# Kernel tuning notes

Measured on AMD Instinct MI355X. Metric: run time of the kernel, lower is better.

Reference implementation:

```python
import jax, jax.numpy as jnp
import numpy as np
from jax import lax

DT = 1.0 / 120.0      # system dt from SystemModel(dt=1/120)
G = 9.81              # gravity for friction force
K_SIGN = 100.0        # smooth sign() sharpness (tanh surrogate, differentiable)
TWO_PI = 2.0 * np.pi


def setup_inputs() -> dict:
    key = jax.random.key(0)
    k1, k2, k3, k4 = jax.random.split(key, 4)
    N, T = 8192, 64
    params = jax.random.uniform(k1, (4,), jnp.float32, 0.05, 0.5)           # friction, damping, tableRes, rimFriction
    covariance_params = jax.random.normal(k2, (7,), jnp.float32) * 0.5 - 5.0  # log-variances
    init_state = jax.random.normal(k3, (N, 6), jnp.float32) * 0.5            # [x, y, vx, vy, theta, omega]
    measurements = jax.random.normal(k4, (N, T, 3), jnp.float32) * 0.5       # [x, y, theta] per step
    return {"params": params, "covariance_params": covariance_params,
            "init_state": init_state, "measurements": measurements}


def reference(params, covariance_params, init_state, measurements):
    """Batched EKF over N segments (vectorized over the Python segment loop of the
    original) with lax.scan over the segment_size timesteps. Returns the mean
    log-likelihood loss: mean over segments of sum_t 0.5*(logdet(S_t) + y_t^T S_t^{-1} y_t),
    with the +-2*pi angle-wrap on the theta innovation as in the original."""
    dyna = jnp.abs(params)
    fric, damp = dyna[0], dyna[1]

    cp = covariance_params
    R = jnp.diag(jnp.exp(cp[:3]))                                            # 3x3 measurement noise
    Q = jnp.diag(jnp.exp(jnp.stack([cp[3], cp[3], cp[4], cp[4], cp[5], cp[6]])))  # 6x6 process noise

    N = init_state.shape[0]
    P0 = jnp.broadcast_to(jnp.eye(6, dtype=init_state.dtype) * 0.01, (N, 6, 6))
    midx = jnp.array([0, 1, 4])
    H = jnp.zeros((3, 6), init_state.dtype).at[0, 0].set(1.).at[1, 1].set(1.).at[2, 4].set(1.)
    I6 = jnp.eye(6, dtype=init_state.dtype)

    def predict(x):
        # free-slide puck dynamics: damping + dry friction (smooth sign)
        pos, vel, th, om = x[:, 0:2], x[:, 2:4], x[:, 4], x[:, 5]
        t = jnp.tanh(K_SIGN * vel)
        pos_n = pos + DT * vel
        vel_n = vel - DT * (damp * vel + fric * G * t)
        th_n = th + DT * om
        om_n = om - DT * damp * om
        return jnp.concatenate([pos_n, vel_n, th_n[:, None], om_n[:, None]], axis=1), t

    def jacobian_F(t):
        # analytic Jacobian of predict; [N,6,6]
        N_ = t.shape[0]
        dv = 1.0 - DT * (damp + fric * G * K_SIGN * (1.0 - t * t))           # [N,2]
        F = jnp.broadcast_to(I6, (N_, 6, 6))
        F = F.at[:, 0, 2].set(DT).at[:, 1, 3].set(DT).at[:, 4, 5].set(DT)
        F = F.at[:, 2, 2].set(dv[:, 0]).at[:, 3, 3].set(dv[:, 1])
        F = F.at[:, 5, 5].set(1.0 - DT * damp)
        return F

    def step(carry, z):
        x, P = carry
        x_pred, t = predict(x)
        F = jacobian_F(t)
        P_pred = jnp.einsum('nij,njk,nlk->nil', F, P, F) + Q                  # F P F^T + Q

        y = z - x_pred[:, midx]                                               # innovation [N,3]
        ang = y[:, 2]
        ang = jnp.where(ang > 1.5 * np.pi, ang - TWO_PI,
                        jnp.where(ang < -1.5 * np.pi, ang + TWO_PI, ang))
        y = y.at[:, 2].set(ang)

        S = P_pred[:, midx, :][:, :, midx] + R                                # [N,3,3]
        Sinv = jnp.linalg.inv(S)
        K = jnp.einsum('nij,njk->nik', P_pred[:, :, midx], Sinv)              # [N,6,3]

        x_new = x_pred + jnp.einsum('nij,nj->ni', K, y)
        KH = jnp.einsum('nij,jk->nik', K, H)                                  # [N,6,6]
        P_new = jnp.einsum('nij,njk->nik', I6 - KH, P_pred)

        _, logdet = jnp.linalg.slogdet(S)
        maha = jnp.einsum('ni,nij,nj->n', y, Sinv, y)
        loss_t = 0.5 * jnp.sum(logdet + maha)
        return (x_new, P_new), loss_t

    (_, _), losses = lax.scan(step, (init_state, P0),
                              jnp.transpose(measurements, (1, 0, 2)))        # scan over T
    return jnp.sum(losses) / N
```

## Files before the change

### kernel.cpp

```cpp
#include <hip/hip_runtime.h>
#include <math.h>

#define DT_STEP (1.0f / 120.0f)
#define G_ACC 9.81f
#define KS 100.0f

__device__ __forceinline__ float frcp(float x) { return __builtin_amdgcn_rcpf(x); }

template <int FT>
__device__ __forceinline__ void ekf_step(
    const float damp, const float fG, const float a55,
    const float R, const float Qp, const float Qv,
    float& s0, float& s1, float& a, float& b, float& c,
    const float z, float& maha, float& sprod)
{
    const float PI15 = 4.7123889803846899f;
    const float TWOPI = 6.2831853071795865f;

    float s0p, s1p, dv;
    if constexpr (FT < 2) {
        const float e = __expf(2.0f * KS * s1);
        const float u = 2.0f * frcp(e + 1.0f);
        const float th = 1.0f - u;
        s0p = fmaf(DT_STEP, s1, s0);
        s1p = s1 - DT_STEP * fmaf(damp, s1, fG * th);
        dv = 1.0f - DT_STEP * fmaf(fG * KS, u * (2.0f - u), damp);
    } else {
        s0p = fmaf(DT_STEP, s1, s0);
        s1p = a55 * s1;
        dv = a55;
    }

    const float M00 = fmaf(DT_STEP, b, a);
    const float M01 = fmaf(DT_STEP, c, b);
    const float Pp00 = fmaf(DT_STEP, M01, M00) + Qp;
    const float Pp01 = dv * M01;
    const float Pp11 = fmaf(dv * dv, c, Qv);

    float y = z - s0p;
    if constexpr (FT == 2) {
        if (y > PI15) y -= TWOPI;
        else if (y < -PI15) y += TWOPI;
    }

    const float S = Pp00 + R;
    const float Si = frcp(S);
    const float K0 = Pp00 * Si;
    const float K1 = Pp01 * Si;

    s0 = fmaf(K0, y, s0p);
    s1 = fmaf(K1, y, s1p);

    const float omk = 1.0f - K0;
    a = Pp00 * omk;
    b = Pp01 * omk;
    c = fmaf(-K1, Pp01, Pp11);

    maha = fmaf(y * y, Si, maha);
    sprod *= S;
}

template <int TT, int FT>
__device__ __forceinline__ float run_filter(
    const float damp, const float fG, const float a55,
    const float R, const float Qp, const float Qv,
    float s0, float s1, const float (&z)[TT])
{
    float a = 0.01f, b = 0.0f, c = 0.01f;
    float maha = 0.0f, logsum = 0.0f;
    static_assert(TT % 8 == 0, "TT multiple of 8");
#pragma unroll
    for (int g = 0; g < TT / 8; g++) {
        float sprod = 1.0f;
#pragma unroll
        for (int k = 0; k < 8; k++)
            ekf_step<FT>(damp, fG, a55, R, Qp, Qv, s0, s1, a, b, c, z[g * 8 + k], maha, sprod);
        logsum += __logf(sprod);
    }
    return logsum + maha;
}

template <int TT>
__global__ __launch_bounds__(64, 1) void ekf_reg_kernel(
    const float* __restrict__ params, const float* __restrict__ cp,
    const float* __restrict__ init_state, const float* __restrict__ meas,
    float* __restrict__ out, int N)
{
    const int lane = threadIdx.x & 63;
    const int seg = blockIdx.x * 64 + lane;
    const int ft = blockIdx.y;
    float local = 0.0f;

    if (seg < N) {
        const float* zrow = meas + (size_t)seg * (3 * TT) + ft;
        float z[TT];
#pragma unroll
        for (int t = 0; t < TT; t++) z[t] = zrow[3 * t];

        const float fric = fabsf(params[0]);
        const float damp = fabsf(params[1]);
        const float fG = fric * G_ACC;
        const float a55 = 1.0f - DT_STEP * damp;

        const float R  = __expf(cp[ft]);
        const float Qp = __expf((ft == 2) ? cp[5] : cp[3]);
        const float Qv = __expf((ft == 2) ? cp[6] : cp[4]);

        const float* sb = init_state + (size_t)seg * 6;
        const float s0 = sb[(ft == 2) ? 4 : ft];
        const float s1 = sb[(ft == 2) ? 5 : ft + 2];

        if (ft == 0)      local = run_filter<TT, 0>(damp, fG, a55, R, Qp, Qv, s0, s1, z);
        else if (ft == 1) local = run_filter<TT, 1>(damp, fG, a55, R, Qp, Qv, s0, s1, z);
        else              local = run_filter<TT, 2>(damp, fG, a55, R, Qp, Qv, s0, s1, z);
    }

#pragma unroll
    for (int off = 32; off > 0; off >>= 1)
        local += __shfl_down(local, off, 64);

    if (lane == 0) atomicAdd(out, local * 0.5f / (float)N);
}

__global__ __launch_bounds__(64, 1) void ekf_gen_kernel(
    const float* __restrict__ params, const float* __restrict__ cp,
    const float* __restrict__ init_state, const float* __restrict__ meas,
    float* __restrict__ out, int N, int T)
{
    const int lane = threadIdx.x & 63;
    const int seg = blockIdx.x * 64 + lane;
    const int ft = blockIdx.y;
    float local = 0.0f;

    if (seg < N) {
        const float fric = fabsf(params[0]);
        const float damp = fabsf(params[1]);
        const float fG = fric * G_ACC;
        const float a55 = 1.0f - DT_STEP * damp;
        const float R  = __expf(cp[ft]);
        const float Qp = __expf((ft == 2) ? cp[5] : cp[3]);
        const float Qv = __expf((ft == 2) ? cp[6] : cp[4]);
        const float* sb = init_state + (size_t)seg * 6;
        float s0 = sb[(ft == 2) ? 4 : ft];
        float s1 = sb[(ft == 2) ? 5 : ft + 2];
        float a = 0.01f, b = 0.0f, c = 0.01f;
        float maha = 0.0f, logsum = 0.0f;

        const float* zrow = meas + (size_t)seg * (3 * T) + ft;
        for (int t = 0; t < T; t++) {
            float sprod = 1.0f;
            const float z = zrow[3 * t];
            if (ft == 0)      ekf_step<0>(damp, fG, a55, R, Qp, Qv, s0, s1, a, b, c, z, maha, sprod);
            else if (ft == 1) ekf_step<1>(damp, fG, a55, R, Qp, Qv, s0, s1, a, b, c, z, maha, sprod);
            else              ekf_step<2>(damp, fG, a55, R, Qp, Qv, s0, s1, a, b, c, z, maha, sprod);
            logsum += __logf(sprod);
        }
        local = logsum + maha;
    }

#pragma unroll
    for (int off = 32; off > 0; off >>= 1)
        local += __shfl_down(local, off, 64);
    if (lane == 0) atomicAdd(out, local * 0.5f / (float)N);
}

extern "C" void kernel_launch(void* const* d_in, const int* in_sizes, int n_in,
                              void* d_out, int out_size, void* d_ws, size_t ws_size,
                              hipStream_t stream) {
    const float* params     = (const float*)d_in[0];
    const float* cov_params = (const float*)d_in[1];
    const float* init_state = (const float*)d_in[2];
    const float* meas       = (const float*)d_in[3];
    float* out = (float*)d_out;

    const int N = in_sizes[2] / 6;
    const int T = in_sizes[3] / (N * 3);

    dim3 grid((N + 63) / 64, 3);
    if (T == 64) {
        ekf_reg_kernel<64><<<grid, 64, 0, stream>>>(params, cov_params, init_state, meas, out, N);
    } else {
        hipMemsetAsync(out, 0, sizeof(float), stream);
        ekf_gen_kernel<<<grid, 64, 0, stream>>>(params, cov_params, init_state, meas, out, N, T);
    }
}
```

Before: 74.03 us.

## Pack x/y filters into two-wide float vectors and split grid by axis

The x and y position filters were two separate blocks. They now run in one thread using two-wide float vectors, so the arithmetic can map to packed FMA instructions, while the theta filter runs in its own block. The grid goes from three blocks per segment group to two. The covariance update is also simplified algebraically to a = R*K0 and b = R*K1, which saves a subtraction. In exchange, each x/y thread carries a longer serial chain with twice the live registers, and the transcendental calls stay scalar.

```diff
diff --git a/kernel.cpp b/kernel.cpp
--- a/kernel.cpp
+++ b/kernel.cpp
@@ -5,31 +5,66 @@
 #define G_ACC 9.81f
 #define KS 100.0f
 
+typedef float v2f __attribute__((ext_vector_type(2)));
+
 __device__ __forceinline__ float frcp(float x) { return __builtin_amdgcn_rcpf(x); }
-
-template <int FT>
-__device__ __forceinline__ void ekf_step(
-    const float damp, const float fG, const float a55,
-    const float R, const float Qp, const float Qv,
+__device__ __forceinline__ v2f fma2(v2f a, v2f b, v2f c) { return __builtin_elementwise_fma(a, b, c); }
+
+__device__ __forceinline__ void ekf_step_pk(
+    const float damp, const float fG, const float fGKS,
+    const v2f R, const float Qp, const float Qv,
+    v2f& s0, v2f& s1, v2f& a, v2f& b, v2f& c,
+    const v2f z, v2f& maha, v2f& sprod)
+{
+    v2f e;
+    e.x = __expf(2.0f * KS * s1.x);
+    e.y = __expf(2.0f * KS * s1.y);
+    v2f u;
+    u.x = 2.0f * frcp(e.x + 1.0f);
+    u.y = 2.0f * frcp(e.y + 1.0f);
+    const v2f th = 1.0f - u;
+
+    const v2f s0p = fma2((v2f)DT_STEP, s1, s0);
+    const v2f s1p = s1 - DT_STEP * fma2((v2f)damp, s1, fG * th);
+    const v2f dv = 1.0f - DT_STEP * fma2((v2f)fGKS, u * (2.0f - u), (v2f)damp);
+
+    const v2f M00 = fma2((v2f)DT_STEP, b, a);
+    const v2f M01 = fma2((v2f)DT_STEP, c, b);
+    const v2f Pp00 = fma2((v2f)DT_STEP, M01, M00) + Qp;
+    const v2f Pp01 = dv * M01;
+    const v2f Pp11 = fma2(dv * dv, c, (v2f)Qv);
+
+    const v2f y = z - s0p;
+
+    const v2f S = Pp00 + R;
+    v2f Si;
+    Si.x = frcp(S.x);
+    Si.y = frcp(S.y);
+    const v2f K0 = Pp00 * Si;
+    const v2f K1 = Pp01 * Si;
+
+    s0 = fma2(K0, y, s0p);
+    s1 = fma2(K1, y, s1p);
+
+    a = R * K0;
+    b = R * K1;
+    c = fma2(-K1, Pp01, Pp11);
+
+    maha = fma2(y * y, Si, maha);
+    sprod *= S;
+}
+
+__device__ __forceinline__ void ekf_step_th(
+    const float a55, const float R, const float Qp, const float Qv,
     float& s0, float& s1, float& a, float& b, float& c,
     const float z, float& maha, float& sprod)
 {
     const float PI15 = 4.7123889803846899f;
     const float TWOPI = 6.2831853071795865f;
 
-    float s0p, s1p, dv;
-    if constexpr (FT < 2) {
-        const float e = __expf(2.0f * KS * s1);
-        const float u = 2.0f * frcp(e + 1.0f);
-        const float th = 1.0f - u;
-        s0p = fmaf(DT_STEP, s1, s0);
-        s1p = s1 - DT_STEP * fmaf(damp, s1, fG * th);
-        dv = 1.0f - DT_STEP * fmaf(fG * KS, u * (2.0f - u), damp);
-    } else {
-        s0p = fmaf(DT_STEP, s1, s0);
-        s1p = a55 * s1;
-        dv = a55;
-    }
+    const float s0p = fmaf(DT_STEP, s1, s0);
+    const float s1p = a55 * s1;
+    const float dv = a55;
 
     const float M00 = fmaf(DT_STEP, b, a);
     const float M01 = fmaf(DT_STEP, c, b);
@@ -38,10 +73,8 @@
     const float Pp11 = fmaf(dv * dv, c, Qv);
 
     float y = z - s0p;
-    if constexpr (FT == 2) {
-        if (y > PI15) y -= TWOPI;
-        else if (y < -PI15) y += TWOPI;
-    }
+    if (y > PI15) y -= TWOPI;
+    else if (y < -PI15) y += TWOPI;
 
     const float S = Pp00 + R;
     const float Si = frcp(S);
@@ -51,40 +84,97 @@
     s0 = fmaf(K0, y, s0p);
     s1 = fmaf(K1, y, s1p);
 
-    const float omk = 1.0f - K0;
-    a = Pp00 * omk;
-    b = Pp01 * omk;
+    a = R * K0;
+    b = R * K1;
     c = fmaf(-K1, Pp01, Pp11);
 
     maha = fmaf(y * y, Si, maha);
     sprod *= S;
 }
 
-template <int TT, int FT>
-__device__ __forceinline__ float run_filter(
-    const float damp, const float fG, const float a55,
-    const float R, const float Qp, const float Qv,
-    float s0, float s1, const float (&z)[TT])
-{
-    float a = 0.01f, b = 0.0f, c = 0.01f;
-    float maha = 0.0f, logsum = 0.0f;
-    static_assert(TT % 8 == 0, "TT multiple of 8");
-#pragma unroll
-    for (int g = 0; g < TT / 8; g++) {
-        float sprod = 1.0f;
-#pragma unroll
-        for (int k = 0; k < 8; k++)
-            ekf_step<FT>(damp, fG, a55, R, Qp, Qv, s0, s1, a, b, c, z[g * 8 + k], maha, sprod);
-        logsum += __logf(sprod);
-    }
-    return logsum + maha;
-}
-
 template <int TT>
-__global__ __launch_bounds__(64, 1) void ekf_reg_kernel(
+__global__ __launch_bounds__(64, 1) void ekf_pk_kernel(
     const float* __restrict__ params, const float* __restrict__ cp,
     const float* __restrict__ init_state, const float* __restrict__ meas,
     float* __restrict__ out, int N)
+{
+    const int lane = threadIdx.x & 63;
+    const int seg = blockIdx.x * 64 + lane;
+    float local = 0.0f;
+
+    const float fric = fabsf(params[0]);
+    const float damp = fabsf(params[1]);
+    const float* zrow = meas + (size_t)seg * (3 * TT);
+    const float* sb = init_state + (size_t)seg * 6;
+
+    if (blockIdx.y == 0) {
+        v2f z2[TT];
+#pragma unroll
+        for (int t = 0; t < TT; t++) {
+            z2[t].x = zrow[3 * t + 0];
+            z2[t].y = zrow[3 * t + 1];
+        }
+
+        const float fG = fric * G_ACC;
+        const float fGKS = fG * KS;
+        v2f R;
+        R.x = __expf(cp[0]);
+        R.y = __expf(cp[1]);
+        const float Qp = __expf(cp[3]);
+        const float Qv = __expf(cp[4]);
+
+        v2f s0, s1;
+        s0.x = sb[0]; s0.y = sb[1];
+        s1.x = sb[2]; s1.y = sb[3];
+        v2f a = 0.01f, b = (v2f)0.0f, c = 0.01f;
+        v2f maha = (v2f)0.0f;
+        float logsum = 0.0f;
+
+        static_assert(TT % 8 == 0, "TT multiple of 8");
+#pragma unroll
+        for (int g = 0; g < TT / 8; g++) {
+            v2f sprod = 1.0f;
+#pragma unroll
+            for (int k = 0; k < 8; k++)
+                ekf_step_pk(damp, fG, fGKS, R, Qp, Qv, s0, s1, a, b, c, z2[g * 8 + k], maha, sprod);
+            logsum += __logf(sprod.x) + __logf(sprod.y);
+        }
+        local = logsum + maha.x + maha.y;
+    } else {
+        float z[TT];
+#pragma unroll
+        for (int t = 0; t < TT; t++) z[t] = zrow[3 * t + 2];
+
+        const float a55 = 1.0f - DT_STEP * damp;
+        const float R = __expf(cp[2]);
+        const float Qp = __expf(cp[5]);
+        const float Qv = __expf(cp[6]);
+
+        float s0 = sb[4], s1 = sb[5];
+        float a = 0.01f, b = 0.0f, c = 0.01f;
+        float maha = 0.0f, logsum = 0.0f;
+#pragma unroll
+        for (int g = 0; g < TT / 8; g++) {
+            float sprod = 1.0f;
+#pragma unroll
+            for (int k = 0; k < 8; k++)
+                ekf_step_th(a55, R, Qp, Qv, s0, s1, a, b, c, z[g * 8 + k], maha, sprod);
+            logsum += __logf(sprod);
+        }
+        local = logsum + maha;
+    }
+
+#pragma unroll
+    for (int off = 32; off > 0; off >>= 1)
+        local += __shfl_down(local, off, 64);
+
+    if (lane == 0) atomicAdd(out, local * 0.5f / (float)N);
+}
+
+__global__ __launch_bounds__(64, 1) void ekf_gen_kernel(
+    const float* __restrict__ params, const float* __restrict__ cp,
+    const float* __restrict__ init_state, const float* __restrict__ meas,
+    float* __restrict__ out, int N, int T)
 {
     const int lane = threadIdx.x & 63;
     const int seg = blockIdx.x * 64 + lane;
@@ -92,50 +182,10 @@
     float local = 0.0f;
 
     if (seg < N) {
-        const float* zrow = meas + (size_t)seg * (3 * TT) + ft;
-        float z[TT];
-#pragma unroll
-        for (int t = 0; t < TT; t++) z[t] = zrow[3 * t];
-
         const float fric = fabsf(params[0]);
         const float damp = fabsf(params[1]);
         const float fG = fric * G_ACC;
-        const float a55 = 1.0f - DT_STEP * damp;
-
-        const float R  = __expf(cp[ft]);
-        const float Qp = __expf((ft == 2) ? cp[5] : cp[3]);
-        const float Qv = __expf((ft == 2) ? cp[6] : cp[4]);
-
-        const float* sb = init_state + (size_t)seg * 6;
-        const float s0 = sb[(ft == 2) ? 4 : ft];
-        const float s1 = sb[(ft == 2) ? 5 : ft + 2];
-
-        if (ft == 0)      local = run_filter<TT, 0>(damp, fG, a55, R, Qp, Qv, s0, s1, z);
-        else if (ft == 1) local = run_filter<TT, 1>(damp, fG, a55, R, Qp, Qv, s0, s1, z);
-        else              local = run_filter<TT, 2>(damp, fG, a55, R, Qp, Qv, s0, s1, z);
-    }
-
-#pragma unroll
-    for (int off = 32; off > 0; off >>= 1)
-        local += __shfl_down(local, off, 64);
-
-    if (lane == 0) atomicAdd(out, local * 0.5f / (float)N);
-}
-
-__global__ __launch_bounds__(64, 1) void ekf_gen_kernel(
-    const float* __restrict__ params, const float* __restrict__ cp,
-    const float* __restrict__ init_state, const float* __restrict__ meas,
-    float* __restrict__ out, int N, int T)
-{
-    const int lane = threadIdx.x & 63;
-    const int seg = blockIdx.x * 64 + lane;
-    const int ft = blockIdx.y;
-    float local = 0.0f;
-
-    if (seg < N) {
-        const float fric = fabsf(params[0]);
-        const float damp = fabsf(params[1]);
-        const float fG = fric * G_ACC;
+        const float fGKS = fG * KS;
         const float a55 = 1.0f - DT_STEP * damp;
         const float R  = __expf(cp[ft]);
         const float Qp = __expf((ft == 2) ? cp[5] : cp[3]);
@@ -150,9 +200,15 @@
         for (int t = 0; t < T; t++) {
             float sprod = 1.0f;
             const float z = zrow[3 * t];
-            if (ft == 0)      ekf_step<0>(damp, fG, a55, R, Qp, Qv, s0, s1, a, b, c, z, maha, sprod);
-            else if (ft == 1) ekf_step<1>(damp, fG, a55, R, Qp, Qv, s0, s1, a, b, c, z, maha, sprod);
-            else              ekf_step<2>(damp, fG, a55, R, Qp, Qv, s0, s1, a, b, c, z, maha, sprod);
+            if (ft == 2) {
+                ekf_step_th(a55, R, Qp, Qv, s0, s1, a, b, c, z, maha, sprod);
+            } else {
+                v2f s0v = (v2f)s0, s1v = (v2f)s1, av = (v2f)a, bv = (v2f)b, cv = (v2f)c;
+                v2f mv = (v2f)0.0f, sp = (v2f)1.0f;
+                ekf_step_pk(damp, fG, fGKS, (v2f)R, Qp, Qv, s0v, s1v, av, bv, cv, (v2f)z, mv, sp);
+                s0 = s0v.x; s1 = s1v.x; a = av.x; b = bv.x; c = cv.x;
+                maha += mv.x; sprod *= sp.x;
+            }
             logsum += __logf(sprod);
         }
         local = logsum + maha;
@@ -176,11 +232,12 @@
     const int N = in_sizes[2] / 6;
     const int T = in_sizes[3] / (N * 3);
 
-    dim3 grid((N + 63) / 64, 3);
-    if (T == 64) {
-        ekf_reg_kernel<64><<<grid, 64, 0, stream>>>(params, cov_params, init_state, meas, out, N);
+    if (T == 64 && (N % 64) == 0) {
+        dim3 grid(N / 64, 2);
+        ekf_pk_kernel<64><<<grid, 64, 0, stream>>>(params, cov_params, init_state, meas, out, N);
     } else {
         hipMemsetAsync(out, 0, sizeof(float), stream);
+        dim3 grid((N + 63) / 64, 3);
         ekf_gen_kernel<<<grid, 64, 0, stream>>>(params, cov_params, init_state, meas, out, N, T);
     }
 }
```

Result: faster. 72.09 us (-2.6%).
